# Optimization experiments

Measured on AMD Instinct MI355X. Metric: run time of the kernel, lower is better.

Reference implementation:

```python
import jax, jax.numpy as jnp
import numpy as np

N_NODES = 50000
N_EDGES = 800000
D_FEAT = 128      # node feature dim
D_IN = 2 * D_FEAT # MLP input (concat of x_i and x_j - x_i)
D_OUT = 256


def setup_inputs() -> dict:
    key = jax.random.key(0)
    ks = jax.random.split(key, 8)
    x = jax.random.normal(ks[0], (N_NODES, D_FEAT), dtype=jnp.float32)
    edge_index = jax.random.randint(ks[1], (2, N_EDGES), 0, N_NODES, dtype=jnp.int64)
    s1 = 1.0 / np.sqrt(D_IN)
    s2 = 1.0 / np.sqrt(D_OUT)
    W1 = jax.random.uniform(ks[2], (D_IN, D_OUT), jnp.float32, -s1, s1)
    b1 = jax.random.uniform(ks[3], (D_OUT,), jnp.float32, -s1, s1)
    W2 = jax.random.uniform(ks[4], (D_OUT, D_OUT), jnp.float32, -s2, s2)
    b2 = jax.random.uniform(ks[5], (D_OUT,), jnp.float32, -s2, s2)
    W3 = jax.random.uniform(ks[6], (D_OUT, D_OUT), jnp.float32, -s2, s2)
    b3 = jax.random.uniform(ks[7], (D_OUT,), jnp.float32, -s2, s2)
    return {"x": x, "edge_index": edge_index, "W1": W1, "b1": b1,
            "W2": W2, "b2": b2, "W3": W3, "b3": b3}


def reference(x, edge_index, W1, b1, W2, b2, W3, b3):
    # EdgeConv: for edge (j -> i): msg = MLP(concat([x_i, x_j - x_i])); max-aggregate at i
    src, dst = edge_index[0], edge_index[1]
    x_i = x[dst]                       # [E, D_FEAT] target features
    x_j = x[src]                       # [E, D_FEAT] source features
    e = jnp.concatenate([x_i, x_j - x_i], axis=-1)  # [E, 2*D_FEAT]
    h = jax.nn.relu(e @ W1 + b1)
    h = jax.nn.relu(h @ W2 + b2)
    h = h @ W3 + b3                    # [E, D_OUT]
    out = jax.ops.segment_max(h, dst, num_segments=N_NODES)  # [N, D_OUT]
    # nodes with no incoming edges -> 0 (PyG scatter-max fill)
    return jnp.where(jnp.isfinite(out), out, jnp.zeros((), out.dtype))
```

## Files before the change

kernel.cpp:

```cpp
#include <hip/hip_runtime.h>
#include <stdint.h>


#define N_NODES 50000
#define N_EDGES 800000

typedef __attribute__((ext_vector_type(4))) float f32x4;
typedef __attribute__((ext_vector_type(8))) _Float16 f16x8;
typedef __attribute__((ext_vector_type(4))) unsigned int u32x4;
typedef __attribute__((ext_vector_type(2))) unsigned int u32x2;

__device__ __forceinline__ unsigned int pkrtz(float a, float b){
  auto p = __builtin_amdgcn_cvt_pkrtz(a, b);
  return __builtin_bit_cast(unsigned int, p);
}
__device__ __forceinline__ unsigned int f16bits(float f){
  _Float16 h = (_Float16)f;
  return (unsigned int)__builtin_bit_cast(unsigned short, h);
}
__device__ __forceinline__ unsigned int pkadd_relu(unsigned int a, unsigned int b){
  unsigned int s, r;
  asm("v_pk_add_f16 %0, %1, %2" : "=v"(s) : "v"(a), "v"(b));
  asm("v_pk_max_f16 %0, %1, %2" : "=v"(r) : "v"(s), "v"(0u));
  return r;
}
__device__ __forceinline__ unsigned int fmap(float f){
  unsigned int u = __builtin_bit_cast(unsigned int, f);
  return (u & 0x80000000u) ? ~u : (u | 0x80000000u);
}
__device__ __forceinline__ bool is64(const unsigned int* e){
  return (e[1] | e[3] | e[5] | e[7] | e[9] | e[11] | e[13] | e[15]) == 0u;
}

extern "C" __global__ void k_hist(const void* __restrict__ eidx, unsigned int* __restrict__ cnt){
  int i = blockIdx.x * 256 + threadIdx.x;
  int d = is64((const unsigned int*)eidx)
        ? (int)((const long long*)eidx)[N_EDGES + i]
        : ((const int*)eidx)[N_EDGES + i];
  atomicAdd(&cnt[d], 1u);
}

extern "C" __global__ void __launch_bounds__(1024) k_scan(const unsigned int* __restrict__ cnt,
                                                          unsigned int* __restrict__ off){
  __shared__ unsigned int ps[1024];
  const int t = threadIdx.x;
  const int lo = t * 49;
  const int hi = (lo + 49 < N_NODES) ? lo + 49 : N_NODES;
  unsigned int s = 0;
  for (int i = lo; i < hi; i++) s += cnt[i];
  ps[t] = s; __syncthreads();
  for (int d = 1; d < 1024; d <<= 1){
    unsigned int v = (t >= d) ? ps[t - d] : 0u;
    __syncthreads();
    ps[t] += v;
    __syncthreads();
  }
  unsigned int run = (t > 0) ? ps[t - 1] : 0u;
  for (int i = lo; i < hi; i++){ off[i] = run; run += cnt[i]; }
}

extern "C" __global__ void k_bucket(const void* __restrict__ eidx,
                                    unsigned int* __restrict__ cur, unsigned int* __restrict__ sPair){
  int i = blockIdx.x * 256 + threadIdx.x;
  int s, d;
  if (is64((const unsigned int*)eidx)){
    const long long* p = (const long long*)eidx;
    s = (int)p[i]; d = (int)p[N_EDGES + i];
  } else {
    const int* p = (const int*)eidx;
    s = p[i]; d = p[N_EDGES + i];
  }
  unsigned int pos = atomicAdd(&cur[d], 1u);
  sPair[pos] = (unsigned int)s | ((unsigned int)d << 16);
}

extern "C" __global__ void k_wprep(const float* __restrict__ W1, const float* __restrict__ W2,
                                   const float* __restrict__ W3,
                                   unsigned short* __restrict__ w2s, unsigned short* __restrict__ w3s,
                                   unsigned short* __restrict__ wdf){
  int t = blockIdx.x * 256 + threadIdx.x;
  if (t < 16384){
    const float* W = (t & 8192) ? W3 : W2;
    unsigned short* o = (t & 8192) ? w3s : w2s;
    int r = t & 8191, lane = r & 63, blk = r >> 6;
    int m  = (blk >> 3) * 16 + (lane & 15);
    int k0 = (blk & 7) * 32 + (lane >> 4) * 8;
    u32x4 ov;
    #pragma unroll
    for (int j = 0; j < 4; j++){
      unsigned int lo = f16bits(W[(size_t)(k0 + 2*j    ) * 256 + m]);
      unsigned int hi = f16bits(W[(size_t)(k0 + 2*j + 1) * 256 + m]);
      ov[j] = lo | (hi << 16);
    }
    *(u32x4*)(o + (size_t)r * 8) = ov;
  } else {
    int r = t - 16384, lane = r & 63, blk = r >> 6;
    int m  = (blk >> 2) * 16 + (lane & 15);
    int k0 = (blk & 3) * 32 + (lane >> 4) * 8;
    u32x4 ov;
    #pragma unroll
    for (int j = 0; j < 4; j++){
      float vlo, vhi;
      int ka = k0 + 2*j, kb = k0 + 2*j + 1;
      if (m < 256){
        vlo = W1[(size_t)ka * 256 + m] - W1[(size_t)(ka + 128) * 256 + m];
        vhi = W1[(size_t)kb * 256 + m] - W1[(size_t)(kb + 128) * 256 + m];
      } else {
        vlo = W1[(size_t)(ka + 128) * 256 + (m - 256)];
        vhi = W1[(size_t)(kb + 128) * 256 + (m - 256)];
      }
      ov[j] = f16bits(vlo) | (f16bits(vhi) << 16);
    }
    *(u32x4*)(wdf + (size_t)r * 8) = ov;
  }
}

extern "C" __global__ void __launch_bounds__(256) k_acm(
    const float* __restrict__ x, const unsigned short* __restrict__ wdf,
    const float* __restrict__ b1, unsigned short* __restrict__ acb){
  __shared__ unsigned char smx[16384];
  const int tid = threadIdx.x, lane = tid & 63, w = tid >> 6;
  const int n0 = blockIdx.x * 64;
  {
    const int nl = tid >> 2, q = tid & 3;
    int node = n0 + nl; if (node > N_NODES - 1) node = N_NODES - 1;
    const f32x4* xp = (const f32x4*)(x + (size_t)node * 128 + q * 32);
    unsigned char* base = smx + (((nl >> 4) * 256 + q * 64 + (nl & 15)) << 4);
    #pragma unroll
    for (int s = 0; s < 4; s++){
      f32x4 v0 = xp[s * 2], v1 = xp[s * 2 + 1];
      u32x4 ov = { pkrtz(v0[0], v0[1]), pkrtz(v0[2], v0[3]),
                   pkrtz(v1[0], v1[1]), pkrtz(v1[2], v1[3]) };
      *(u32x4*)(base + s * 256) = ov;
    }
  }
  __syncthreads();
  const int lm = lane & 15, g = lane >> 4;
  f32x4 acc[8][4];
  #pragma unroll
  for (int mf = 0; mf < 8; mf++)
    #pragma unroll
    for (int nf = 0; nf < 4; nf++) acc[mf][nf] = (f32x4){0.f, 0.f, 0.f, 0.f};
  #pragma unroll
  for (int ks = 0; ks < 4; ks++){
    f16x8 af[8], bfr[4];
    #pragma unroll
    for (int mf = 0; mf < 8; mf++)
      af[mf] = __builtin_bit_cast(f16x8, *(const u32x4*)(wdf + (size_t)(((w * 8 + mf) * 4 + ks) * 64 + lane) * 8));
    #pragma unroll
    for (int nf = 0; nf < 4; nf++)
      bfr[nf] = __builtin_bit_cast(f16x8, *(const u32x4*)(smx + nf * 4096 + ks * 1024 + lane * 16));
    #pragma unroll
    for (int mf = 0; mf < 8; mf++)
      #pragma unroll
      for (int nf = 0; nf < 4; nf++)
        acc[mf][nf] = __builtin_amdgcn_mfma_f32_16x16x32_f16(af[mf], bfr[nf], acc[mf][nf], 0, 0, 0);
  }
  #pragma unroll
  for (int mf = 0; mf < 8; mf++){
    const int m0 = w * 128 + mf * 16 + g * 4;
    f32x4 bb = (f32x4){0.f, 0.f, 0.f, 0.f};
    if (w < 2) bb = *(const f32x4*)(b1 + m0);
    #pragma unroll
    for (int nf = 0; nf < 4; nf++){
      int node = n0 + nf * 16 + lm;
      if (node < N_NODES){
        u32x2 pv = { pkrtz(acc[mf][nf][0] + bb[0], acc[mf][nf][1] + bb[1]),
                     pkrtz(acc[mf][nf][2] + bb[2], acc[mf][nf][3] + bb[3]) };
        *(u32x2*)(acb + (size_t)node * 512 + m0) = pv;
      }
    }
  }
}

extern "C" __global__ void __launch_bounds__(256, 4) k_edge(
    const unsigned short* __restrict__ acb,
    const unsigned short* __restrict__ w2f, const unsigned short* __restrict__ w3f,
    const float* __restrict__ b2, const float* __restrict__ b3,
    const unsigned int* __restrict__ sPair,
    unsigned int* __restrict__ outu){
  __shared__ unsigned char sm[32768];
  __shared__ int dstI[64];
  __shared__ int srcI[64];
  const int tid = threadIdx.x;
  const int lane = tid & 63;
  const int w = tid >> 6;

  const int bid = blockIdx.x;
  const int xcd = bid & 7, idx = bid >> 3;
  const int sb = (xcd < 4) ? xcd * 1563 : 4 * 1563 + (xcd - 4) * 1562;
  const int e0 = (sb + idx) * 64;

  f16x8 afp[4];
  #pragma unroll
  for (int mf = 0; mf < 4; mf++)
    afp[mf] = __builtin_bit_cast(f16x8, *(const u32x4*)(w2f + (size_t)(((w * 4 + mf) * 8 + 0) * 64 + lane) * 8));

  if (tid < 64){
    unsigned int pr = sPair[e0 + tid];
    srcI[tid] = (int)(pr & 0xFFFFu);
    dstI[tid] = (int)(pr >> 16);
  }
  __syncthreads();

  {
    const int e = tid >> 2, q = tid & 3;
    const unsigned short* pa = acb + (size_t)dstI[e] * 512 + q * 64;
    const unsigned short* pc = acb + (size_t)srcI[e] * 512 + 256 + q * 64;
    unsigned char* base = sm + (e >> 4) * 8192 + (e & 15) * 16;
    #pragma unroll
    for (int j = 0; j < 8; j++){
      u32x4 ua = *(const u32x4*)(pa + j * 8);
      u32x4 uc = *(const u32x4*)(pc + j * 8);
      u32x4 ov;
      #pragma unroll
      for (int t2 = 0; t2 < 4; t2++) ov[t2] = pkadd_relu(ua[t2], uc[t2]);
      *(u32x4*)(base + (q * 2 + (j >> 2)) * 1024 + (j & 3) * 256) = ov;
    }
  }
  __syncthreads();

  const int lm = lane & 15, g = lane >> 4;
  f32x4 acc[4][4];
  #pragma unroll
  for (int mf = 0; mf < 4; mf++)
    #pragma unroll
    for (int nf = 0; nf < 4; nf++) acc[mf][nf] = (f32x4){0.f, 0.f, 0.f, 0.f};

  #pragma unroll
  for (int ks = 0; ks < 8; ks++){
    f16x8 af[4], bfr[4];
    #pragma unroll
    for (int mf = 0; mf < 4; mf++)
      af[mf] = (ks == 0) ? afp[mf]
             : __builtin_bit_cast(f16x8, *(const u32x4*)(w2f + (size_t)(((w * 4 + mf) * 8 + ks) * 64 + lane) * 8));
    #pragma unroll
    for (int nf = 0; nf < 4; nf++)
      bfr[nf] = __builtin_bit_cast(f16x8, *(const u32x4*)(sm + nf * 8192 + ks * 1024 + lane * 16));
    __builtin_amdgcn_s_setprio(1);
    #pragma unroll
    for (int mf = 0; mf < 4; mf++)
      #pragma unroll
      for (int nf = 0; nf < 4; nf++)
        acc[mf][nf] = __builtin_amdgcn_mfma_f32_16x16x32_f16(af[mf], bfr[nf], acc[mf][nf], 0, 0, 0);
    __builtin_amdgcn_s_setprio(0);
  }

  #pragma unroll
  for (int mf = 0; mf < 4; mf++)
    afp[mf] = __builtin_bit_cast(f16x8, *(const u32x4*)(w3f + (size_t)(((w * 4 + mf) * 8 + 0) * 64 + lane) * 8));
  __syncthreads();

  {
    #pragma unroll
    for (int mf = 0; mf < 4; mf++){
      const int m0 = w * 64 + mf * 16 + g * 4;
      const f32x4 bb = *(const f32x4*)(b2 + m0);
      const int boff = (m0 >> 5) * 1024 + ((m0 >> 3) & 3) * 256 + lm * 16 + (m0 & 7) * 2;
      #pragma unroll
      for (int nf = 0; nf < 4; nf++){
        float v0 = fmaxf(acc[mf][nf][0] + bb[0], 0.f);
        float v1 = fmaxf(acc[mf][nf][1] + bb[1], 0.f);
        float v2 = fmaxf(acc[mf][nf][2] + bb[2], 0.f);
        float v3 = fmaxf(acc[mf][nf][3] + bb[3], 0.f);
        u32x2 pv = { pkrtz(v0, v1), pkrtz(v2, v3) };
        *(u32x2*)(sm + nf * 8192 + boff) = pv;
      }
    }
  }
  __syncthreads();

  #pragma unroll
  for (int mf = 0; mf < 4; mf++)
    #pragma unroll
    for (int nf = 0; nf < 4; nf++) acc[mf][nf] = (f32x4){0.f, 0.f, 0.f, 0.f};
  #pragma unroll
  for (int ks = 0; ks < 8; ks++){
    f16x8 af[4], bfr[4];
    #pragma unroll
    for (int mf = 0; mf < 4; mf++)
      af[mf] = (ks == 0) ? afp[mf]
             : __builtin_bit_cast(f16x8, *(const u32x4*)(w3f + (size_t)(((w * 4 + mf) * 8 + ks) * 64 + lane) * 8));
    #pragma unroll
    for (int nf = 0; nf < 4; nf++)
      bfr[nf] = __builtin_bit_cast(f16x8, *(const u32x4*)(sm + nf * 8192 + ks * 1024 + lane * 16));
    __builtin_amdgcn_s_setprio(1);
    #pragma unroll
    for (int mf = 0; mf < 4; mf++)
      #pragma unroll
      for (int nf = 0; nf < 4; nf++)
        acc[mf][nf] = __builtin_amdgcn_mfma_f32_16x16x32_f16(af[mf], bfr[nf], acc[mf][nf], 0, 0, 0);
    __builtin_amdgcn_s_setprio(0);
  }
  __syncthreads();

  float vmaxf = -__builtin_inff();
  int curDst = dstI[0];
  const int t4 = tid * 4;
  #pragma unroll
  for (int half = 0; half < 2; half++){
    #pragma unroll
    for (int mf = 0; mf < 4; mf++){
      const int m0 = w * 64 + mf * 16 + g * 4;
      const f32x4 bb = *(const f32x4*)(b3 + m0);
      #pragma unroll
      for (int nfl = 0; nfl < 2; nfl++){
        const int r = nfl * 16 + lm;
        const int nf = half * 2 + nfl;
        f32x4 v = { acc[mf][nf][0] + bb[0], acc[mf][nf][1] + bb[1],
                    acc[mf][nf][2] + bb[2], acc[mf][nf][3] + bb[3] };
        *(f32x4*)(sm + r * 1024 + ((m0 * 4) ^ ((r & 7) << 4))) = v;
      }
    }
    __syncthreads();
    for (int it = 0; it < 32; it++){
      float v = *(const float*)(sm + it * 1024 + (t4 ^ ((it & 7) << 4)));
      const int d = dstI[half * 32 + it];
      if (d != curDst){
        atomicMax(outu + (size_t)curDst * 256 + tid, fmap(vmaxf));
        curDst = d; vmaxf = -__builtin_inff();
      }
      vmaxf = fmaxf(vmaxf, v);
    }
    __syncthreads();
  }
  atomicMax(outu + (size_t)curDst * 256 + tid, fmap(vmaxf));
}

extern "C" __global__ void k_fix(u32x4* __restrict__ o){
  size_t i = (size_t)blockIdx.x * 256 + threadIdx.x;
  u32x4 u = o[i];
  #pragma unroll
  for (int j = 0; j < 4; j++)
    u[j] = (u[j] == 0u) ? 0u : ((u[j] & 0x80000000u) ? (u[j] ^ 0x80000000u) : ~u[j]);
  o[i] = u;
}

extern "C" void kernel_launch(void* const* d_in, const int* in_sizes, int n_in,
                              void* d_out, int out_size, void* d_ws, size_t ws_size,
                              hipStream_t stream){
  const float* x  = (const float*)d_in[0];
  const void*  ei = d_in[1];
  const float* W1 = (const float*)d_in[2];
  const float* b1 = (const float*)d_in[3];
  const float* W2 = (const float*)d_in[4];
  const float* b2 = (const float*)d_in[5];
  const float* W3 = (const float*)d_in[6];
  const float* b3 = (const float*)d_in[7];

  const size_t AC_BYTES = (size_t)N_NODES * 512 * 2;
  const size_t W_BYTES  = 256 * 256 * 2;
  const size_t P_BYTES  = (size_t)N_EDGES * 4;
  const size_t C_BYTES  = 200704;
  char* ws = (char*)d_ws;
  size_t o = 0;
  unsigned short* acb  = (unsigned short*)(ws + o); o += AC_BYTES;
  unsigned short* w2s  = (unsigned short*)(ws + o); o += W_BYTES;
  unsigned short* w3s  = (unsigned short*)(ws + o); o += W_BYTES;
  unsigned short* wdf  = (unsigned short*)(ws + o); o += W_BYTES;
  unsigned int*  sPair = (unsigned int*)(ws + o);   o += P_BYTES;
  unsigned int*  cnt   = (unsigned int*)(ws + o);   o += C_BYTES;
  unsigned int*  offA  = (unsigned int*)(ws + o);   o += C_BYTES;
  if (ws_size < o) return;

  (void)hipMemsetAsync(cnt, 0, C_BYTES, stream);
  k_hist<<<N_EDGES / 256, 256, 0, stream>>>(ei, cnt);
  k_scan<<<1, 1024, 0, stream>>>(cnt, offA);
  k_bucket<<<N_EDGES / 256, 256, 0, stream>>>(ei, offA, sPair);
  k_wprep<<<96, 256, 0, stream>>>(W1, W2, W3, w2s, w3s, wdf);
  k_acm<<<(N_NODES + 63) / 64, 256, 0, stream>>>(x, wdf, b1, acb);
  (void)hipMemsetAsync(d_out, 0, (size_t)out_size * 4, stream);
  k_edge<<<N_EDGES / 64, 256, 0, stream>>>(acb, w2s, w3s, b2, b3, sPair, (unsigned int*)d_out);
  k_fix<<<out_size / 1024, 256, 0, stream>>>((u32x4*)d_out);
}
```

Measured before the change: 524.2 us.

## Shrink edge tile to 48 edges for occupancy and parallelize offset scan

The edge MLP kernel now processes 48 edges per workgroup instead of 64. That cuts the accumulator registers and shared memory, so launch bounds can target 6 workgroups per CU instead of 4. The XCD-aware block mapping and the tail clamping are adjusted to match. The single-block serial prefix scan over node counts is replaced by a three-kernel multi-block scan. The trade-off is less weight reuse per workgroup, more blocks, more atomics at tile boundaries, and extra kernel launches.

```diff
diff --git a/kernel.cpp b/kernel.cpp
--- a/kernel.cpp
+++ b/kernel.cpp
@@ -4,6 +4,8 @@
 
 #define N_NODES 50000
 #define N_EDGES 800000
+#define EPB 48
+#define NBLK 16667
 
 typedef __attribute__((ext_vector_type(4))) float f32x4;
 typedef __attribute__((ext_vector_type(8))) _Float16 f16x8;
@@ -40,23 +42,40 @@
   atomicAdd(&cnt[d], 1u);
 }
 
-extern "C" __global__ void __launch_bounds__(1024) k_scan(const unsigned int* __restrict__ cnt,
-                                                          unsigned int* __restrict__ off){
-  __shared__ unsigned int ps[1024];
+extern "C" __global__ void k_psum(const unsigned int* __restrict__ cnt, unsigned int* __restrict__ bsum){
+  __shared__ unsigned int red[4];
+  const int b = blockIdx.x, t = threadIdx.x, i = b * 256 + t;
+  unsigned int v = (i < N_NODES) ? cnt[i] : 0u;
+  #pragma unroll
+  for (int d = 32; d; d >>= 1) v += __shfl_down(v, d, 64);
+  if ((t & 63) == 0) red[t >> 6] = v;
+  __syncthreads();
+  if (t == 0) bsum[b] = red[0] + red[1] + red[2] + red[3];
+}
+extern "C" __global__ void __launch_bounds__(256) k_bscan(const unsigned int* __restrict__ bsum,
+                                                          unsigned int* __restrict__ bbase){
+  __shared__ unsigned int s[256];
   const int t = threadIdx.x;
-  const int lo = t * 49;
-  const int hi = (lo + 49 < N_NODES) ? lo + 49 : N_NODES;
-  unsigned int s = 0;
-  for (int i = lo; i < hi; i++) s += cnt[i];
-  ps[t] = s; __syncthreads();
-  for (int d = 1; d < 1024; d <<= 1){
-    unsigned int v = (t >= d) ? ps[t - d] : 0u;
-    __syncthreads();
-    ps[t] += v;
-    __syncthreads();
-  }
-  unsigned int run = (t > 0) ? ps[t - 1] : 0u;
-  for (int i = lo; i < hi; i++){ off[i] = run; run += cnt[i]; }
+  unsigned int v = (t < 196) ? bsum[t] : 0u;
+  s[t] = v; __syncthreads();
+  for (int d = 1; d < 256; d <<= 1){
+    unsigned int u = (t >= d) ? s[t - d] : 0u;
+    __syncthreads(); s[t] += u; __syncthreads();
+  }
+  if (t < 196) bbase[t] = s[t] - v;
+}
+extern "C" __global__ void k_apply(const unsigned int* __restrict__ cnt,
+                                   const unsigned int* __restrict__ bbase,
+                                   unsigned int* __restrict__ off){
+  __shared__ unsigned int s[256];
+  const int b = blockIdx.x, t = threadIdx.x, i = b * 256 + t;
+  unsigned int v = (i < N_NODES) ? cnt[i] : 0u;
+  s[t] = v; __syncthreads();
+  for (int d = 1; d < 256; d <<= 1){
+    unsigned int u = (t >= d) ? s[t - d] : 0u;
+    __syncthreads(); s[t] += u; __syncthreads();
+  }
+  if (i < N_NODES) off[i] = bbase[b] + s[t] - v;
 }
 
 extern "C" __global__ void k_bucket(const void* __restrict__ eidx,
@@ -173,37 +192,38 @@
   }
 }
 
-extern "C" __global__ void __launch_bounds__(256, 4) k_edge(
+extern "C" __global__ void __launch_bounds__(256, 6) k_edge(
     const unsigned short* __restrict__ acb,
     const unsigned short* __restrict__ w2f, const unsigned short* __restrict__ w3f,
     const float* __restrict__ b2, const float* __restrict__ b3,
     const unsigned int* __restrict__ sPair,
     unsigned int* __restrict__ outu){
-  __shared__ unsigned char sm[32768];
-  __shared__ int dstI[64];
-  __shared__ int srcI[64];
+  __shared__ unsigned char sm[24576];
+  __shared__ int dstI[EPB];
+  __shared__ int srcI[EPB];
   const int tid = threadIdx.x;
   const int lane = tid & 63;
   const int w = tid >> 6;
 
   const int bid = blockIdx.x;
   const int xcd = bid & 7, idx = bid >> 3;
-  const int sb = (xcd < 4) ? xcd * 1563 : 4 * 1563 + (xcd - 4) * 1562;
-  const int e0 = (sb + idx) * 64;
+  const int wgid = ((xcd < 3) ? xcd * 2084 : 3 * 2084 + (xcd - 3) * 2083) + idx;
+  const int e0 = wgid * EPB;
 
   f16x8 afp[4];
   #pragma unroll
   for (int mf = 0; mf < 4; mf++)
     afp[mf] = __builtin_bit_cast(f16x8, *(const u32x4*)(w2f + (size_t)(((w * 4 + mf) * 8 + 0) * 64 + lane) * 8));
 
-  if (tid < 64){
-    unsigned int pr = sPair[e0 + tid];
+  if (tid < EPB){
+    int eg = e0 + tid; if (eg > N_EDGES - 1) eg = N_EDGES - 1;
+    unsigned int pr = sPair[eg];
     srcI[tid] = (int)(pr & 0xFFFFu);
     dstI[tid] = (int)(pr >> 16);
   }
   __syncthreads();
 
-  {
+  if (tid < EPB * 4){
     const int e = tid >> 2, q = tid & 3;
     const unsigned short* pa = acb + (size_t)dstI[e] * 512 + q * 64;
     const unsigned short* pc = acb + (size_t)srcI[e] * 512 + 256 + q * 64;
@@ -221,27 +241,27 @@
   __syncthreads();
 
   const int lm = lane & 15, g = lane >> 4;
-  f32x4 acc[4][4];
+  f32x4 acc[4][3];
   #pragma unroll
   for (int mf = 0; mf < 4; mf++)
     #pragma unroll
-    for (int nf = 0; nf < 4; nf++) acc[mf][nf] = (f32x4){0.f, 0.f, 0.f, 0.f};
+    for (int nf = 0; nf < 3; nf++) acc[mf][nf] = (f32x4){0.f, 0.f, 0.f, 0.f};
 
   #pragma unroll
   for (int ks = 0; ks < 8; ks++){
-    f16x8 af[4], bfr[4];
+    f16x8 af[4], bfr[3];
     #pragma unroll
     for (int mf = 0; mf < 4; mf++)
       af[mf] = (ks == 0) ? afp[mf]
              : __builtin_bit_cast(f16x8, *(const u32x4*)(w2f + (size_t)(((w * 4 + mf) * 8 + ks) * 64 + lane) * 8));
     #pragma unroll
-    for (int nf = 0; nf < 4; nf++)
+    for (int nf = 0; nf < 3; nf++)
       bfr[nf] = __builtin_bit_cast(f16x8, *(const u32x4*)(sm + nf * 8192 + ks * 1024 + lane * 16));
     __builtin_amdgcn_s_setprio(1);
     #pragma unroll
     for (int mf = 0; mf < 4; mf++)
       #pragma unroll
-      for (int nf = 0; nf < 4; nf++)
+      for (int nf = 0; nf < 3; nf++)
         acc[mf][nf] = __builtin_amdgcn_mfma_f32_16x16x32_f16(af[mf], bfr[nf], acc[mf][nf], 0, 0, 0);
     __builtin_amdgcn_s_setprio(0);
   }
@@ -258,7 +278,7 @@
       const f32x4 bb = *(const f32x4*)(b2 + m0);
       const int boff = (m0 >> 5) * 1024 + ((m0 >> 3) & 3) * 256 + lm * 16 + (m0 & 7) * 2;
       #pragma unroll
-      for (int nf = 0; nf < 4; nf++){
+      for (int nf = 0; nf < 3; nf++){
         float v0 = fmaxf(acc[mf][nf][0] + bb[0], 0.f);
         float v1 = fmaxf(acc[mf][nf][1] + bb[1], 0.f);
         float v2 = fmaxf(acc[mf][nf][2] + bb[2], 0.f);
@@ -273,22 +293,22 @@
   #pragma unroll
   for (int mf = 0; mf < 4; mf++)
     #pragma unroll
-    for (int nf = 0; nf < 4; nf++) acc[mf][nf] = (f32x4){0.f, 0.f, 0.f, 0.f};
+    for (int nf = 0; nf < 3; nf++) acc[mf][nf] = (f32x4){0.f, 0.f, 0.f, 0.f};
   #pragma unroll
   for (int ks = 0; ks < 8; ks++){
-    f16x8 af[4], bfr[4];
+    f16x8 af[4], bfr[3];
     #pragma unroll
     for (int mf = 0; mf < 4; mf++)
       af[mf] = (ks == 0) ? afp[mf]
              : __builtin_bit_cast(f16x8, *(const u32x4*)(w3f + (size_t)(((w * 4 + mf) * 8 + ks) * 64 + lane) * 8));
     #pragma unroll
-    for (int nf = 0; nf < 4; nf++)
+    for (int nf = 0; nf < 3; nf++)
       bfr[nf] = __builtin_bit_cast(f16x8, *(const u32x4*)(sm + nf * 8192 + ks * 1024 + lane * 16));
     __builtin_amdgcn_s_setprio(1);
     #pragma unroll
     for (int mf = 0; mf < 4; mf++)
       #pragma unroll
-      for (int nf = 0; nf < 4; nf++)
+      for (int nf = 0; nf < 3; nf++)
         acc[mf][nf] = __builtin_amdgcn_mfma_f32_16x16x32_f16(af[mf], bfr[nf], acc[mf][nf], 0, 0, 0);
     __builtin_amdgcn_s_setprio(0);
   }
@@ -298,24 +318,19 @@
   int curDst = dstI[0];
   const int t4 = tid * 4;
   #pragma unroll
-  for (int half = 0; half < 2; half++){
+  for (int third = 0; third < 3; third++){
     #pragma unroll
     for (int mf = 0; mf < 4; mf++){
       const int m0 = w * 64 + mf * 16 + g * 4;
       const f32x4 bb = *(const f32x4*)(b3 + m0);
-      #pragma unroll
-      for (int nfl = 0; nfl < 2; nfl++){
-        const int r = nfl * 16 + lm;
-        const int nf = half * 2 + nfl;
-        f32x4 v = { acc[mf][nf][0] + bb[0], acc[mf][nf][1] + bb[1],
-                    acc[mf][nf][2] + bb[2], acc[mf][nf][3] + bb[3] };
-        *(f32x4*)(sm + r * 1024 + ((m0 * 4) ^ ((r & 7) << 4))) = v;
-      }
+      f32x4 v = { acc[mf][third][0] + bb[0], acc[mf][third][1] + bb[1],
+                  acc[mf][third][2] + bb[2], acc[mf][third][3] + bb[3] };
+      *(f32x4*)(sm + lm * 1024 + ((m0 * 4) ^ ((lm & 7) << 4))) = v;
     }
     __syncthreads();
-    for (int it = 0; it < 32; it++){
+    for (int it = 0; it < 16; it++){
       float v = *(const float*)(sm + it * 1024 + (t4 ^ ((it & 7) << 4)));
-      const int d = dstI[half * 32 + it];
+      const int d = dstI[third * 16 + it];
       if (d != curDst){
         atomicMax(outu + (size_t)curDst * 256 + tid, fmap(vmaxf));
         curDst = d; vmaxf = -__builtin_inff();
@@ -361,15 +376,19 @@
   unsigned int*  sPair = (unsigned int*)(ws + o);   o += P_BYTES;
   unsigned int*  cnt   = (unsigned int*)(ws + o);   o += C_BYTES;
   unsigned int*  offA  = (unsigned int*)(ws + o);   o += C_BYTES;
+  unsigned int*  bsum  = (unsigned int*)(ws + o);   o += 1024;
+  unsigned int*  bbase = (unsigned int*)(ws + o);   o += 1024;
   if (ws_size < o) return;
 
   (void)hipMemsetAsync(cnt, 0, C_BYTES, stream);
   k_hist<<<N_EDGES / 256, 256, 0, stream>>>(ei, cnt);
-  k_scan<<<1, 1024, 0, stream>>>(cnt, offA);
+  k_psum<<<196, 256, 0, stream>>>(cnt, bsum);
+  k_bscan<<<1, 256, 0, stream>>>(bsum, bbase);
+  k_apply<<<196, 256, 0, stream>>>(cnt, bbase, offA);
   k_bucket<<<N_EDGES / 256, 256, 0, stream>>>(ei, offA, sPair);
   k_wprep<<<96, 256, 0, stream>>>(W1, W2, W3, w2s, w3s, wdf);
   k_acm<<<(N_NODES + 63) / 64, 256, 0, stream>>>(x, wdf, b1, acb);
   (void)hipMemsetAsync(d_out, 0, (size_t)out_size * 4, stream);
-  k_edge<<<N_EDGES / 64, 256, 0, stream>>>(acb, w2s, w3s, b2, b3, sPair, (unsigned int*)d_out);
+  k_edge<<<NBLK, 256, 0, stream>>>(acb, w2s, w3s, b2, b3, sPair, (unsigned int*)d_out);
   k_fix<<<out_size / 1024, 256, 0, stream>>>((u32x4*)d_out);
 }
```

Result: slower. 1.267 ms (+141.8%).
